# Kernel optimization log

Measured on AMD Instinct MI355X. Metric: run time of the kernel, lower is better.

Reference implementation:

```python
import jax, jax.numpy as jnp
import numpy as np

# Model dims
B, N, D_MODEL, N_HEADS = 8, 4096, 512, 8
EXPAND = 2
D1 = (EXPAND * D_MODEL) // N_HEADS * N_HEADS      # 1024
HEAD_DIM = D1 // N_HEADS                          # 128
RANK, NK = 32, 16
GAMMA = 0.999


def setup_inputs() -> dict:
    key = jax.random.key(0)
    ks = jax.random.split(key, 24)

    def p(i, shape, std=0.02):
        return std * jax.random.normal(ks[i], shape, dtype=jnp.float32)

    def toep_params(i0):
        # SKI low-rank Toeplitz operator params: kernel values at NK inducing
        # lag positions, factorized as (h, nk, r) @ (h, r, d), plus lag-0 term.
        return (p(i0, (N_HEADS, 1, HEAD_DIM), 1.0),        # zero lag
                p(i0 + 1, (N_HEADS, NK, RANK), 0.1),       # pos lags A
                p(i0 + 2, (N_HEADS, RANK, HEAD_DIM), 0.1), # pos lags B
                p(i0 + 3, (N_HEADS, NK, RANK), 0.1),       # neg lags A
                p(i0 + 4, (N_HEADS, RANK, HEAD_DIM), 0.1)) # neg lags B

    t1 = toep_params(7)
    t2 = toep_params(12)
    return {
        'x': jax.random.normal(ks[0], (B, N, D_MODEL), dtype=jnp.float32),
        'u_w': p(1, (D1, D_MODEL)), 'u_b': p(2, (D1,)),
        'v_w': p(3, (D1, D_MODEL)), 'v_b': p(4, (D1,)),
        'o_w': p(5, (D_MODEL, D1)), 'o_b': p(6, (D_MODEL,)),
        't1_zero': t1[0], 't1_pa': t1[1], 't1_pb': t1[2], 't1_na': t1[3], 't1_nb': t1[4],
        't2_zero': t2[0], 't2_pa': t2[1], 't2_pb': t2[2], 't2_na': t2[3], 't2_nb': t2[4],
    }


def _build_kernel(zero, pos_a, pos_b, neg_a, neg_b, n):
    """Build circular-conv kernel a of shape (h, 2n, d): a[k]=t(k), a[2n-k]=t(-k)."""
    h, nk, _ = pos_a.shape
    d = pos_b.shape[-1]
    tm_pos = jnp.einsum('hkr,hrd->hkd', pos_a, pos_b)   # kernel at inducing lags
    tm_neg = jnp.einsum('hkr,hrd->hkd', neg_a, neg_b)
    lags = jnp.arange(1, n, dtype=jnp.float32)          # lags 1..n-1
    # linear interpolation from NK inducing points to n-1 lags
    pos_f = (lags - 1.0) / max(n - 2, 1) * (nk - 1)
    lo = jnp.floor(pos_f).astype(jnp.int32)
    hi = jnp.minimum(lo + 1, nk - 1)
    w = (pos_f - lo)[None, :, None]
    decay = (GAMMA ** lags)[None, :, None]              # exponential decay bias
    t_pos = ((1.0 - w) * tm_pos[:, lo] + w * tm_pos[:, hi]) * decay
    t_neg = ((1.0 - w) * tm_neg[:, lo] + w * tm_neg[:, hi]) * decay
    return jnp.concatenate(
        [zero, t_pos, jnp.zeros((h, 1, d), t_pos.dtype), jnp.flip(t_neg, axis=1)],
        axis=1)


def _toep_apply(x, zero, pos_a, pos_b, neg_a, neg_b):
    # x: (b, n, g) with g = h*d; multi-head Toeplitz mixing along axis 1 via FFT.
    b, n, g = x.shape
    h = zero.shape[0]
    d = g // h
    xh = x.reshape(b, n, h, d).transpose(0, 2, 1, 3)    # (b, h, n, d)
    a = _build_kernel(zero, pos_a, pos_b, neg_a, neg_b, n)  # (h, 2n, d)
    y = jnp.fft.irfft(
        jnp.fft.rfft(xh, 2 * n, axis=2) * jnp.fft.rfft(a, axis=1)[None],
        2 * n, axis=2)[:, :, :n]
    return y.transpose(0, 2, 1, 3).reshape(b, n, g)


def reference(x, u_w, u_b, v_w, v_b, o_w, o_b,
              t1_zero, t1_pa, t1_pb, t1_na, t1_nb,
              t2_zero, t2_pa, t2_pb, t2_na, t2_nb):
    b, n, _ = x.shape
    H = int(np.sqrt(n))
    W = n // H
    u = jax.nn.silu(x @ u_w.T + u_b)
    v = jax.nn.silu(x @ v_w.T + v_b)
    g = v.shape[-1]
    t1 = (t1_zero, t1_pa, t1_pb, t1_na, t1_nb)
    t2 = (t2_zero, t2_pa, t2_pb, t2_na, t2_nb)
    # path 1: mix along W (rows) with toep1, then along H (cols) with toep2
    o1 = _toep_apply(v.reshape(b * H, W, g), *t1)
    o1 = o1.reshape(b, H, W, g).transpose(0, 2, 1, 3).reshape(b * W, H, g)
    o1 = _toep_apply(o1, *t2)
    o1 = o1.reshape(b, W, H, g).transpose(0, 2, 1, 3).reshape(b, H * W, g)
    # path 2: mix along H with toep2, then along W with toep1
    v2 = v.reshape(b, H, W, g).transpose(0, 2, 1, 3).reshape(b * W, H, g)
    o2 = _toep_apply(v2, *t2)
    o2 = o2.reshape(b, W, H, g).transpose(0, 2, 1, 3).reshape(b * H, W, g)
    o2 = _toep_apply(o2, *t1)
    o2 = o2.reshape(b, H * W, g)
    # SiLU gate + output projection
    return (u * (o1 + o2)) @ o_w.T + o_b
```

## Files before the change

### kernel.cpp

```cpp
#include <hip/hip_runtime.h>
#include <hip/hip_bf16.h>
#include <hip/hip_fp16.h>

typedef __bf16 bf16;
typedef bf16 bf16x2 __attribute__((ext_vector_type(2)));
typedef bf16 bf16x4 __attribute__((ext_vector_type(4)));
typedef bf16 bf16x8 __attribute__((ext_vector_type(8)));
typedef float f32x2 __attribute__((ext_vector_type(2)));
typedef float f32x4 __attribute__((ext_vector_type(4)));

__device__ __forceinline__ void gload_lds16(const void* g, void* l) {
  __builtin_amdgcn_global_load_lds((__attribute__((address_space(1))) void*)g,
                                   (__attribute__((address_space(3))) void*)l,
                                   16, 0, 0);
}

__device__ __forceinline__ f32x2 fma2(f32x2 a, f32x2 b, f32x2 c) {
  return __builtin_elementwise_fma(a, b, c);
}

__device__ __forceinline__ float silu_f(float xv) {
  return xv * __builtin_amdgcn_rcpf(1.f + __expf(-xv));
}


__global__ void cast_f32_to_bf16(const float* __restrict__ in, bf16* __restrict__ out, int n4) {
  int i = blockIdx.x * blockDim.x + threadIdx.x;
  if (i >= n4) return;
  float4 v = ((const float4*)in)[i];
  bf16x4 o = {(bf16)v.x, (bf16)v.y, (bf16)v.z, (bf16)v.w};
  ((bf16x4*)out)[i] = o;
}

__global__ void cast_w3(const float* __restrict__ uw, const float* __restrict__ vw,
                        const float* __restrict__ ow,
                        bf16* __restrict__ wuv, bf16* __restrict__ owb) {
  int t = blockIdx.x * 256 + threadIdx.x;
  int r = t >> 17;
  int i = t & 131071;
  const float* src = (r == 0) ? uw : (r == 1) ? vw : ow;
  bf16* dst = (r == 2) ? owb : (wuv + (r == 1) * 524288);
  float4 v = ((const float4*)src)[i];
  bf16x4 o = {(bf16)v.x, (bf16)v.y, (bf16)v.z, (bf16)v.w};
  ((bf16x4*)dst)[i] = o;
}

__global__ void concat_bias(const float* __restrict__ ub, const float* __restrict__ vb,
                            float* __restrict__ buv) {
  int i = blockIdx.x * blockDim.x + threadIdx.x;
  if (i < 1024) { buv[i] = ub[i]; buv[1024 + i] = vb[i]; }
}

__global__ void build_tkf(const float* __restrict__ zero, const float* __restrict__ pa,
                          const float* __restrict__ pb, const float* __restrict__ na,
                          const float* __restrict__ nb, float* __restrict__ Tkf,
                          float scale) {
  int idx = blockIdx.x * blockDim.x + threadIdx.x;
  if (idx >= 8 * 127 * 128) return;
  int d = idx & 127;
  int lagIdx = (idx >> 7) % 127;
  int h = idx / (128 * 127);
  int lag = lagIdx - 63;
  float val;
  if (lag == 0) {
    val = zero[h * 128 + d];
  } else {
    int k = lag > 0 ? lag : -lag;
    const float* A  = lag > 0 ? pa : na;
    const float* Bm = lag > 0 ? pb : nb;
    float pos_f = (float)(k - 1) * (15.0f / 62.0f);
    int lo = (int)floorf(pos_f);
    int hi = min(lo + 1, 15);
    float w = pos_f - (float)lo;
    float s = 0.f;
    for (int r = 0; r < 32; ++r) {
      float c = (1.f - w) * A[(h * 16 + lo) * 32 + r] + w * A[(h * 16 + hi) * 32 + r];
      s += c * Bm[(h * 32 + r) * 128 + d];
    }
    val = s * powf(0.999f, (float)k);
  }
  Tkf[idx] = val * scale;
}


template<int MODE>
__global__ __launch_bounds__(512, 2)
void gemm8(const bf16* __restrict__ A, const bf16* __restrict__ Bm,
           const float* __restrict__ bias,
           bf16* __restrict__ out_u, bf16* __restrict__ out_v,
           float* __restrict__ out_f, int M, int N, int K) {
  __shared__ __align__(16) char lds[131072];
  const int tid  = threadIdx.x;
  const int lane = tid & 63;
  const int l15  = lane & 15;
  const int lk16 = ((lane >> 4) & 3) << 4;
  const int w    = tid >> 6;
  const int wm   = (w >> 2) << 7;
  const int wn   = (w & 3) << 6;
  const int nbn  = N >> 8;
  const int cpx  = gridDim.x >> 3;
  const int swzb = (blockIdx.x & 7) * cpx + (blockIdx.x >> 3);
  const int br   = (swzb / nbn) << 8;
  const int bc   = (swzb % nbn) << 8;
  const int wub  = __builtin_amdgcn_readfirstlane(tid & 448);
  const int nkt  = K >> 6;

  f32x4 acc[8][4] = {};

  auto stage = [&](int kt, int b) {
    const int k0 = kt << 6;
    char* Al = lds + b * 65536;
    char* Bl = Al + 32768;
#pragma unroll
    for (int g = 0; g < 4; ++g) {
      const int flat = g * 512 + tid;
      const int row  = flat >> 3;
      const int cb   = ((flat & 7) << 4) ^ ((row & 7) << 4);
      gload_lds16((const char*)(A  + (size_t)(br + row) * K + k0) + cb,
                  Al + (g * 512 + wub) * 16);
      gload_lds16((const char*)(Bm + (size_t)(bc + row) * K + k0) + cb,
                  Bl + (g * 512 + wub) * 16);
    }
  };

  stage(0, 0);

  for (int kt = 0; kt < nkt; ++kt) {
    const int b = kt & 1;
    asm volatile("s_waitcnt vmcnt(0)" ::: "memory");
    __builtin_amdgcn_s_barrier();
    __builtin_amdgcn_sched_barrier(0);
    if (kt + 1 < nkt) stage(kt + 1, b ^ 1);

    const char* Ab = lds + b * 65536;
    const char* Bb = Ab + 32768;
#pragma unroll
    for (int ks = 0; ks < 2; ++ks) {
      bf16x8 bfr[4];
#pragma unroll
      for (int n = 0; n < 4; ++n) {
        const int row = wn + n * 16 + l15;
        bfr[n] = *(const bf16x8*)(Bb + row * 128 + (((ks << 6) | lk16) ^ ((row & 7) << 4)));
      }
      __builtin_amdgcn_s_setprio(1);
#pragma unroll
      for (int m = 0; m < 8; ++m) {
        const int row = wm + m * 16 + l15;
        bf16x8 af = *(const bf16x8*)(Ab + row * 128 + (((ks << 6) | lk16) ^ ((row & 7) << 4)));
#pragma unroll
        for (int n = 0; n < 4; ++n)
          acc[m][n] = __builtin_amdgcn_mfma_f32_16x16x32_bf16(af, bfr[n], acc[m][n], 0, 0, 0);
      }
      __builtin_amdgcn_s_setprio(0);
    }
  }

  const int lr4 = ((lane >> 4) & 3) << 2;
  if (MODE == 0) {
    const bool isU = (bc < 1024);
    bf16* outp = isU ? out_u : out_v;
    const int obc = bc & 1023;
#pragma unroll
    for (int m = 0; m < 8; ++m) {
#pragma unroll
      for (int n = 0; n < 4; ++n) {
        const int colg = bc + wn + n * 16 + l15;
        const int ocol = obc + wn + n * 16 + l15;
        const float bv = bias[colg];
#pragma unroll
        for (int r = 0; r < 4; ++r) {
          const int row = br + wm + m * 16 + lr4 + r;
          outp[(size_t)row * 1024 + ocol] = (bf16)silu_f(acc[m][n][r] + bv);
        }
      }
    }
  } else {
#pragma unroll
    for (int m = 0; m < 8; ++m) {
#pragma unroll
      for (int n = 0; n < 4; ++n) {
        const int col = bc + wn + n * 16 + l15;
        const float bv = bias[col];
#pragma unroll
        for (int r = 0; r < 4; ++r) {
          const int row = br + wm + m * 16 + lr4 + r;
          out_f[(size_t)row * N + col] = acc[m][n][r] + bv;
        }
      }
    }
  }
}


#define VROW 130

template<int FUSE>
__global__ __launch_bounds__(256, 3)
void toep_pass(const bf16* __restrict__ in, const float* __restrict__ Tkf,
               const bf16* __restrict__ ufuse, bf16* __restrict__ out,
               int stride_j, int stride_row) {
  __shared__ float vbuf[64 * VROW];
  const int tid    = threadIdx.x;
  const int lane   = tid & 63;
  const int rowIdx = blockIdx.x >> 3;
  const int head   = blockIdx.x & 7;
  const size_t base = (size_t)(rowIdx >> 6) * 4194304
                    + (size_t)(rowIdx & 63) * stride_row + head * 128;

  const int i0 = (tid >> 6) << 4;
  const float* tg = Tkf + head * 127 * 128 + (lane << 1);

  f32x2 t[31];
#pragma unroll
  for (int s = 0; s < 31; ++s)
    t[s] = *(const f32x2*)(tg + (i0 + 48 + s) * 128);

#pragma unroll
  for (int it = 0; it < 2; ++it) {
    int c  = it * 256 + tid;
    int j  = c >> 3;
    int cg = c & 7;
    const bf16* p = in + base + (size_t)j * stride_j + cg * 16;
    bf16x8 a0 = *(const bf16x8*)p;
    bf16x8 a1 = *(const bf16x8*)(p + 8);
    f32x4 f0 = {(float)a0[0], (float)a0[1], (float)a0[2], (float)a0[3]};
    f32x4 f1 = {(float)a0[4], (float)a0[5], (float)a0[6], (float)a0[7]};
    f32x4 f2 = {(float)a1[0], (float)a1[1], (float)a1[2], (float)a1[3]};
    f32x4 f3 = {(float)a1[4], (float)a1[5], (float)a1[6], (float)a1[7]};
    float* dst = &vbuf[j * VROW + cg * 16];
    *(f32x4*)(dst)      = f0;
    *(f32x4*)(dst + 4)  = f1;
    *(f32x4*)(dst + 8)  = f2;
    *(f32x4*)(dst + 12) = f3;
  }
  __syncthreads();

  f32x2 acc[16] = {};
#pragma unroll
  for (int jb = 0; jb < 4; ++jb) {
    f32x2 p16[16];
    if (jb < 3) {
#pragma unroll
      for (int s = 0; s < 16; ++s)
        p16[s] = *(const f32x2*)(tg + (i0 - 16 * (jb + 1) + 48 + s) * 128);
    }
#pragma unroll
    for (int jj = 0; jj < 16; ++jj) {
      f32x2 v2 = *(const f32x2*)&vbuf[(jb * 16 + jj) * VROW + (lane << 1)];
#pragma unroll
      for (int ii = 0; ii < 16; ++ii)
        acc[ii] = fma2(t[ii - jj + 15], v2, acc[ii]);
    }
    if (jb < 3) {
#pragma unroll
      for (int s = 30; s >= 16; --s) t[s] = t[s - 16];
#pragma unroll
      for (int s = 0; s < 16; ++s) t[s] = p16[s];
    }
  }

  const int d0 = lane << 1;
#pragma unroll
  for (int ii = 0; ii < 16; ++ii) {
    const size_t oidx = base + (size_t)(i0 + ii) * stride_j + d0;
    float a0 = acc[ii].x, a1 = acc[ii].y;
    if (FUSE) {
      bf16x2 uu = *(const bf16x2*)(ufuse + oidx);
      a0 *= (float)uu[0];
      a1 *= (float)uu[1];
    }
    bf16x2 o2 = {(bf16)a0, (bf16)a1};
    *(bf16x2*)(out + oidx) = o2;
  }
}


extern "C" void kernel_launch(void* const* d_in, const int* in_sizes, int n_in,
                              void* d_out, int out_size, void* d_ws, size_t ws_size,
                              hipStream_t stream) {
  const float* x    = (const float*)d_in[0];
  const float* u_w  = (const float*)d_in[1];
  const float* u_b  = (const float*)d_in[2];
  const float* v_w  = (const float*)d_in[3];
  const float* v_b  = (const float*)d_in[4];
  const float* o_w  = (const float*)d_in[5];
  const float* o_b  = (const float*)d_in[6];
  const float* t1z  = (const float*)d_in[7];
  const float* t1pa = (const float*)d_in[8];
  const float* t1pb = (const float*)d_in[9];
  const float* t1na = (const float*)d_in[10];
  const float* t1nb = (const float*)d_in[11];
  const float* t2z  = (const float*)d_in[12];
  const float* t2pa = (const float*)d_in[13];
  const float* t2pb = (const float*)d_in[14];
  const float* t2na = (const float*)d_in[15];
  const float* t2nb = (const float*)d_in[16];

  char* ws = (char*)d_ws;
  size_t off = 0;
  auto alloc = [&](size_t bytes) {
    char* p = ws + off;
    off += (bytes + 255) & ~(size_t)255;
    return p;
  };
  bf16*  xb   = (bf16*)alloc(32768ull * 512 * 2);
  bf16*  wuv  = (bf16*)alloc(2048ull * 512 * 2);
  bf16*  owb  = (bf16*)alloc(512ull * 1024 * 2);
  float* buv  = (float*)alloc(2048ull * 4);
  float* Tkf1 = (float*)alloc(8ull * 127 * 128 * 4);
  float* Tkf2 = (float*)alloc(8ull * 127 * 128 * 4);
  bf16*  u    = (bf16*)alloc(32768ull * 1024 * 2);
  bf16*  v    = (bf16*)alloc(32768ull * 1024 * 2);
  bf16*  tmid = (bf16*)alloc(32768ull * 1024 * 2);
  bf16*  g    = v;

  cast_f32_to_bf16<<<16384, 256, 0, stream>>>(x, xb, 16777216 / 4);
  cast_w3<<<1536, 256, 0, stream>>>(u_w, v_w, o_w, wuv, owb);
  concat_bias<<<4, 256, 0, stream>>>(u_b, v_b, buv);
  build_tkf<<<508, 256, 0, stream>>>(t1z, t1pa, t1pb, t1na, t1nb, Tkf1, 1.0f);
  build_tkf<<<508, 256, 0, stream>>>(t2z, t2pa, t2pb, t2na, t2nb, Tkf2, 2.0f);

  gemm8<0><<<1024, 512, 0, stream>>>(xb, wuv, buv, u, v, nullptr, 32768, 2048, 512);
  toep_pass<0><<<4096, 256, 0, stream>>>(v, Tkf1, nullptr, tmid, 1024, 65536);
  toep_pass<1><<<4096, 256, 0, stream>>>(tmid, Tkf2, u, g, 65536, 1024);
  gemm8<1><<<256, 512, 0, stream>>>(g, owb, o_b, nullptr, nullptr, (float*)d_out,
                                    32768, 512, 1024);
}
```

Baseline: 286.5 us.

## Fuse x fp32-to-bf16 cast into UV GEMM and stage epilogue through LDS

Removes the standalone cast kernel for x. The UV GEMM now loads fp32 activations into registers, converts them to bf16 and writes them into swizzled LDS, with the register loads overlapped against the MFMA loop. The UV epilogue writes SiLU outputs to LDS first so global stores become 16-byte vectors instead of scattered 2-byte stores. The output GEMM epilogue hoists its bias loads out of the loop. This saves a full read-write of the bf16 copy of x, but GEMM A-loads now read twice as many bytes and go through registers instead of direct-to-LDS loads.

```diff
diff --git a/kernel.cpp b/kernel.cpp
--- a/kernel.cpp
+++ b/kernel.cpp
@@ -23,14 +23,6 @@
   return xv * __builtin_amdgcn_rcpf(1.f + __expf(-xv));
 }
 
-
-__global__ void cast_f32_to_bf16(const float* __restrict__ in, bf16* __restrict__ out, int n4) {
-  int i = blockIdx.x * blockDim.x + threadIdx.x;
-  if (i >= n4) return;
-  float4 v = ((const float4*)in)[i];
-  bf16x4 o = {(bf16)v.x, (bf16)v.y, (bf16)v.z, (bf16)v.w};
-  ((bf16x4*)out)[i] = o;
-}
 
 __global__ void cast_w3(const float* __restrict__ uw, const float* __restrict__ vw,
                         const float* __restrict__ ow,
@@ -83,12 +75,140 @@
 }
 
 
-template<int MODE>
 __global__ __launch_bounds__(512, 2)
-void gemm8(const bf16* __restrict__ A, const bf16* __restrict__ Bm,
-           const float* __restrict__ bias,
-           bf16* __restrict__ out_u, bf16* __restrict__ out_v,
-           float* __restrict__ out_f, int M, int N, int K) {
+void gemm_uv(const float* __restrict__ xf, const bf16* __restrict__ Bm,
+             const float* __restrict__ bias,
+             bf16* __restrict__ out_u, bf16* __restrict__ out_v) {
+  __shared__ __align__(16) char lds[131072];
+  const int K = 512, nkt = 8;
+  const int tid  = threadIdx.x;
+  const int lane = tid & 63;
+  const int l15  = lane & 15;
+  const int lk16 = ((lane >> 4) & 3) << 4;
+  const int w    = tid >> 6;
+  const int wm   = (w >> 2) << 7;
+  const int wn   = (w & 3) << 6;
+  const int cpx  = gridDim.x >> 3;
+  const int swzb = (blockIdx.x & 7) * cpx + (blockIdx.x >> 3);
+  const int br   = (swzb >> 3) << 8;
+  const int bc   = (swzb & 7) << 8;
+  const int wub  = __builtin_amdgcn_readfirstlane(tid & 448);
+
+  f32x4 acc[8][4] = {};
+  float4 va[8];
+
+  auto stageA_load = [&](int kt) {
+    const int k0 = kt << 6;
+#pragma unroll
+    for (int t4 = 0; t4 < 4; ++t4) {
+      const int flat = t4 * 512 + tid;
+      const int row  = flat >> 3;
+      const int c8   = (flat & 7) << 3;
+      const float* p = xf + (size_t)(br + row) * 512 + k0 + c8;
+      va[2 * t4]     = *(const float4*)p;
+      va[2 * t4 + 1] = *(const float4*)(p + 4);
+    }
+  };
+  auto stageA_write = [&](int b) {
+    char* Al = lds + b * 65536;
+#pragma unroll
+    for (int t4 = 0; t4 < 4; ++t4) {
+      const int flat = t4 * 512 + tid;
+      const int row  = flat >> 3;
+      const int cb   = ((flat & 7) << 4) ^ ((row & 7) << 4);
+      float4 a = va[2 * t4], c = va[2 * t4 + 1];
+      bf16x8 o = {(bf16)a.x, (bf16)a.y, (bf16)a.z, (bf16)a.w,
+                  (bf16)c.x, (bf16)c.y, (bf16)c.z, (bf16)c.w};
+      *(bf16x8*)(Al + row * 128 + cb) = o;
+    }
+  };
+  auto stageB = [&](int kt, int b) {
+    const int k0 = kt << 6;
+    char* Bl = lds + b * 65536 + 32768;
+#pragma unroll
+    for (int g = 0; g < 4; ++g) {
+      const int flat = g * 512 + tid;
+      const int row  = flat >> 3;
+      const int cb   = ((flat & 7) << 4) ^ ((row & 7) << 4);
+      gload_lds16((const char*)(Bm + (size_t)(bc + row) * K + k0) + cb,
+                  Bl + (g * 512 + wub) * 16);
+    }
+  };
+
+  stageA_load(0);
+  stageB(0, 0);
+  stageA_write(0);
+
+  for (int kt = 0; kt < nkt; ++kt) {
+    const int b = kt & 1;
+    asm volatile("s_waitcnt vmcnt(0) lgkmcnt(0)" ::: "memory");
+    __builtin_amdgcn_s_barrier();
+    __builtin_amdgcn_sched_barrier(0);
+    if (kt + 1 < nkt) { stageA_load(kt + 1); stageB(kt + 1, b ^ 1); }
+    __builtin_amdgcn_sched_barrier(0);
+
+    const char* Ab = lds + b * 65536;
+    const char* Bb = Ab + 32768;
+#pragma unroll
+    for (int ks = 0; ks < 2; ++ks) {
+      bf16x8 bfr[4];
+#pragma unroll
+      for (int n = 0; n < 4; ++n) {
+        const int row = wn + n * 16 + l15;
+        bfr[n] = *(const bf16x8*)(Bb + row * 128 + (((ks << 6) | lk16) ^ ((row & 7) << 4)));
+      }
+      __builtin_amdgcn_s_setprio(1);
+#pragma unroll
+      for (int m = 0; m < 8; ++m) {
+        const int row = wm + m * 16 + l15;
+        bf16x8 af = *(const bf16x8*)(Ab + row * 128 + (((ks << 6) | lk16) ^ ((row & 7) << 4)));
+#pragma unroll
+        for (int n = 0; n < 4; ++n)
+          acc[m][n] = __builtin_amdgcn_mfma_f32_16x16x32_bf16(af, bfr[n], acc[m][n], 0, 0, 0);
+      }
+      __builtin_amdgcn_s_setprio(0);
+    }
+    __builtin_amdgcn_sched_barrier(0);
+    if (kt + 1 < nkt) stageA_write(b ^ 1);
+  }
+
+  __syncthreads();
+  char* tl = lds + w * 16384;
+  const int lr4 = ((lane >> 4) & 3) << 2;
+#pragma unroll
+  for (int m = 0; m < 8; ++m) {
+#pragma unroll
+    for (int n = 0; n < 4; ++n) {
+      const float bv = bias[bc + wn + n * 16 + l15];
+#pragma unroll
+      for (int r = 0; r < 4; ++r) {
+        const int rr = m * 16 + lr4 + r;
+        const int cc = n * 16 + l15;
+        const int byte = rr * 128 + ((cc * 2) ^ (((rr >> 2) & 3) << 5));
+        *(bf16*)(tl + byte) = (bf16)silu_f(acc[m][n][r] + bv);
+      }
+    }
+  }
+  __syncthreads();
+  const bool isU = (bc < 1024);
+  bf16* outp = isU ? out_u : out_v;
+  const int obc = bc & 1023;
+#pragma unroll
+  for (int i = 0; i < 16; ++i) {
+    const int f   = i * 64 + lane;
+    const int rr  = f >> 3;
+    const int c16 = f & 7;
+    const int byte = rr * 128 + ((c16 * 16) ^ (((rr >> 2) & 3) << 5));
+    bf16x8 vv = *(const bf16x8*)(tl + byte);
+    *(bf16x8*)(outp + (size_t)(br + wm + rr) * 1024 + obc + wn + c16 * 8) = vv;
+  }
+}
+
+
+__global__ __launch_bounds__(512, 2)
+void gemm_o(const bf16* __restrict__ A, const bf16* __restrict__ Bm,
+            const float* __restrict__ bias, float* __restrict__ out_f,
+            int N, int K) {
   __shared__ __align__(16) char lds[131072];
   const int tid  = threadIdx.x;
   const int lane = tid & 63;
@@ -156,37 +276,17 @@
   }
 
   const int lr4 = ((lane >> 4) & 3) << 2;
-  if (MODE == 0) {
-    const bool isU = (bc < 1024);
-    bf16* outp = isU ? out_u : out_v;
-    const int obc = bc & 1023;
-#pragma unroll
-    for (int m = 0; m < 8; ++m) {
-#pragma unroll
-      for (int n = 0; n < 4; ++n) {
-        const int colg = bc + wn + n * 16 + l15;
-        const int ocol = obc + wn + n * 16 + l15;
-        const float bv = bias[colg];
-#pragma unroll
-        for (int r = 0; r < 4; ++r) {
-          const int row = br + wm + m * 16 + lr4 + r;
-          outp[(size_t)row * 1024 + ocol] = (bf16)silu_f(acc[m][n][r] + bv);
-        }
-      }
-    }
-  } else {
-#pragma unroll
-    for (int m = 0; m < 8; ++m) {
-#pragma unroll
-      for (int n = 0; n < 4; ++n) {
-        const int col = bc + wn + n * 16 + l15;
-        const float bv = bias[col];
-#pragma unroll
-        for (int r = 0; r < 4; ++r) {
-          const int row = br + wm + m * 16 + lr4 + r;
-          out_f[(size_t)row * N + col] = acc[m][n][r] + bv;
-        }
-      }
+  float bv[4];
+#pragma unroll
+  for (int n = 0; n < 4; ++n) bv[n] = bias[bc + wn + n * 16 + l15];
+#pragma unroll
+  for (int m = 0; m < 8; ++m) {
+#pragma unroll
+    for (int r = 0; r < 4; ++r) {
+      const int row = br + wm + m * 16 + lr4 + r;
+#pragma unroll
+      for (int n = 0; n < 4; ++n)
+        out_f[(size_t)row * N + bc + wn + n * 16 + l15] = acc[m][n][r] + bv[n];
     }
   }
 }
@@ -303,7 +403,6 @@
     off += (bytes + 255) & ~(size_t)255;
     return p;
   };
-  bf16*  xb   = (bf16*)alloc(32768ull * 512 * 2);
   bf16*  wuv  = (bf16*)alloc(2048ull * 512 * 2);
   bf16*  owb  = (bf16*)alloc(512ull * 1024 * 2);
   float* buv  = (float*)alloc(2048ull * 4);
@@ -314,15 +413,13 @@
   bf16*  tmid = (bf16*)alloc(32768ull * 1024 * 2);
   bf16*  g    = v;
 
-  cast_f32_to_bf16<<<16384, 256, 0, stream>>>(x, xb, 16777216 / 4);
   cast_w3<<<1536, 256, 0, stream>>>(u_w, v_w, o_w, wuv, owb);
   concat_bias<<<4, 256, 0, stream>>>(u_b, v_b, buv);
   build_tkf<<<508, 256, 0, stream>>>(t1z, t1pa, t1pb, t1na, t1nb, Tkf1, 1.0f);
   build_tkf<<<508, 256, 0, stream>>>(t2z, t2pa, t2pb, t2na, t2nb, Tkf2, 2.0f);
 
-  gemm8<0><<<1024, 512, 0, stream>>>(xb, wuv, buv, u, v, nullptr, 32768, 2048, 512);
+  gemm_uv<<<1024, 512, 0, stream>>>(x, wuv, buv, u, v);
   toep_pass<0><<<4096, 256, 0, stream>>>(v, Tkf1, nullptr, tmid, 1024, 65536);
   toep_pass<1><<<4096, 256, 0, stream>>>(tmid, Tkf2, u, g, 65536, 1024);
-  gemm8<1><<<256, 512, 0, stream>>>(g, owb, o_b, nullptr, nullptr, (float*)d_out,
-                                    32768, 512, 1024);
-}
+  gemm_o<<<256, 512, 0, stream>>>(g, owb, o_b, (float*)d_out, 512, 1024);
+}
```

Result: slower. 314.3 us (+9.7%).

## Stage toeplitz input tile as bf16 in LDS via direct global-to-LDS loads

Applied to the files above, without the earlier changes.

The toeplitz pass now copies its 64x128 bf16 input tile straight into LDS with global_load_lds 16-byte transfers instead of loading to registers, converting to fp32 and storing a padded fp32 buffer. The inner loop reads packed bf16 pairs and widens them with shifts. This halves the LDS footprint, which may allow more blocks per CU, and removes the conversion work from the staging phase. The GEMM epilogue is also changed to hoist the bias loads and to reorder the output stores row-major.

```diff
diff --git a/kernel.cpp b/kernel.cpp
--- a/kernel.cpp
+++ b/kernel.cpp
@@ -175,31 +175,29 @@
       }
     }
   } else {
+    float bv[4];
+#pragma unroll
+    for (int n = 0; n < 4; ++n) bv[n] = bias[bc + wn + n * 16 + l15];
 #pragma unroll
     for (int m = 0; m < 8; ++m) {
 #pragma unroll
-      for (int n = 0; n < 4; ++n) {
-        const int col = bc + wn + n * 16 + l15;
-        const float bv = bias[col];
-#pragma unroll
-        for (int r = 0; r < 4; ++r) {
-          const int row = br + wm + m * 16 + lr4 + r;
-          out_f[(size_t)row * N + col] = acc[m][n][r] + bv;
-        }
+      for (int r = 0; r < 4; ++r) {
+        const int row = br + wm + m * 16 + lr4 + r;
+#pragma unroll
+        for (int n = 0; n < 4; ++n)
+          out_f[(size_t)row * N + bc + wn + n * 16 + l15] = acc[m][n][r] + bv[n];
       }
     }
   }
 }
 
-
-#define VROW 130
 
 template<int FUSE>
 __global__ __launch_bounds__(256, 3)
 void toep_pass(const bf16* __restrict__ in, const float* __restrict__ Tkf,
                const bf16* __restrict__ ufuse, bf16* __restrict__ out,
                int stride_j, int stride_row) {
-  __shared__ float vbuf[64 * VROW];
+  __shared__ __align__(16) char vb[16384];
   const int tid    = threadIdx.x;
   const int lane   = tid & 63;
   const int rowIdx = blockIdx.x >> 3;
@@ -215,25 +213,19 @@
   for (int s = 0; s < 31; ++s)
     t[s] = *(const f32x2*)(tg + (i0 + 48 + s) * 128);
 
-#pragma unroll
-  for (int it = 0; it < 2; ++it) {
-    int c  = it * 256 + tid;
-    int j  = c >> 3;
-    int cg = c & 7;
-    const bf16* p = in + base + (size_t)j * stride_j + cg * 16;
-    bf16x8 a0 = *(const bf16x8*)p;
-    bf16x8 a1 = *(const bf16x8*)(p + 8);
-    f32x4 f0 = {(float)a0[0], (float)a0[1], (float)a0[2], (float)a0[3]};
-    f32x4 f1 = {(float)a0[4], (float)a0[5], (float)a0[6], (float)a0[7]};
-    f32x4 f2 = {(float)a1[0], (float)a1[1], (float)a1[2], (float)a1[3]};
-    f32x4 f3 = {(float)a1[4], (float)a1[5], (float)a1[6], (float)a1[7]};
-    float* dst = &vbuf[j * VROW + cg * 16];
-    *(f32x4*)(dst)      = f0;
-    *(f32x4*)(dst + 4)  = f1;
-    *(f32x4*)(dst + 8)  = f2;
-    *(f32x4*)(dst + 12) = f3;
-  }
-  __syncthreads();
+  {
+    const int wub = __builtin_amdgcn_readfirstlane(tid & 192);
+#pragma unroll
+    for (int it = 0; it < 4; ++it) {
+      const int flat = it * 256 + tid;
+      const int row  = flat >> 4;
+      const int c16  = flat & 15;
+      gload_lds16((const char*)(in + base + (size_t)row * stride_j) + c16 * 16,
+                  vb + (it * 256 + wub) * 16);
+    }
+  }
+  asm volatile("s_waitcnt vmcnt(0)" ::: "memory");
+  __builtin_amdgcn_s_barrier();
 
   f32x2 acc[16] = {};
 #pragma unroll
@@ -246,7 +238,10 @@
     }
 #pragma unroll
     for (int jj = 0; jj < 16; ++jj) {
-      f32x2 v2 = *(const f32x2*)&vbuf[(jb * 16 + jj) * VROW + (lane << 1)];
+      unsigned int vu = *(const unsigned int*)(vb + (jb * 16 + jj) * 256 + (lane << 2));
+      f32x2 v2;
+      v2.x = __uint_as_float(vu << 16);
+      v2.y = __uint_as_float(vu & 0xFFFF0000u);
 #pragma unroll
       for (int ii = 0; ii < 16; ++ii)
         acc[ii] = fma2(t[ii - jj + 15], v2, acc[ii]);
```

Result: slower. 365.3 us (+27.5%).
